# Kernel tuning notes

Hardware: AMD Instinct MI355X
Metric: run time of the kernel (lower is better)

## Reference

```python
import jax, jax.numpy as jnp
import numpy as np
from jax import lax

FX, FY = 518.857, 519.469   # NYU-v2 depth intrinsics (cx/cy unused by forward)
B, H, W = 8, 479, 639       # TRAIN_CROP_SIZE = [W, H]; H+1, W+1 divisible by 4
P = 8                       # even PATCH_SIZE -> box-filter output is [H+1, W+1]
EPS = 1e-6


def _coords():
    # u_u0 = x - W/2, v_v0 = y - H/2, broadcast over [B,1,H,W]
    u = jnp.arange(W, dtype=jnp.float32)[None, None, None, :] - W / 2.0
    v = jnp.arange(H, dtype=jnp.float32)[None, None, :, None] - H / 2.0
    return u, v


def _surface_normal(xyz):
    # xyz: [H, W, 3] -> normals [H, W, 3]
    x, y, z = xyz[..., 0], xyz[..., 1], xyz[..., 2]
    # 9 box-filtered moments in a single depthwise conv (the original does 9 conv2d calls)
    mom = jnp.stack([x * x, x * y, x * z, y * y, y * z, z * z, x, y, z], 0)[None]  # [1,9,H,W]
    kern = jnp.ones((9, 1, P, P), xyz.dtype)
    s = lax.conv_general_dilated(mom, kern, (1, 1), [(P // 2, P // 2)] * 2,
                                 feature_group_count=9)[0]  # [9, H+1, W+1]
    xx, xy, xz, yy, yz, zz, xs, ys, zs = s
    ATA = jnp.stack([xx, xy, xz, xy, yy, yz, xz, yz, zz], -1)  # [H+1, W+1, 9]
    Hp, Wp = ATA.shape[0], ATA.shape[1]
    ATA = ATA.reshape(Hp, Wp, 3, 3) + EPS * jnp.eye(3, dtype=xyz.dtype)
    AT1 = jnp.stack([xs, ys, zs], -1)[..., None]  # [H+1, W+1, 3, 1]
    # original loops over 4x4 sub-patches with overlap=0 -> equivalent full-grid solve
    n = jnp.linalg.solve(ATA, AT1)                # [H+1, W+1, 3, 1]
    n = n / jnp.sqrt(jnp.sum(n * n, axis=2, keepdims=True))
    n = n[:-1, :-1, :, 0]                         # [H, W, 3]
    # orient toward camera: flip where dot(n, xyz) > 0
    flip = jnp.sum(n * xyz, axis=2, keepdims=True) > 0
    return jnp.where(flip, -n, n)


def _fit_normals(depth):
    # depth: [B,1,H,W] -> surface normals [B,3,H,W], zeroed where depth <= 0
    u, v = _coords()
    x = u * depth / FX
    y = v * depth / FY
    xyz = jnp.concatenate([x, y, depth], 1).transpose(0, 2, 3, 1)  # [B,H,W,3]
    sn = jax.vmap(_surface_normal)(xyz).transpose(0, 3, 1, 2)      # [B,3,H,W]
    return jnp.where(depth > 0, sn, 0.0)


def setup_inputs() -> dict:
    key = jax.random.key(0)
    k1, k2 = jax.random.split(key)
    prediction = jax.random.uniform(k1, (B, 1, H, W), jnp.float32)
    gt = jax.random.uniform(k2, (B, 1, H, W), jnp.float32)
    return {"prediction": prediction, "gt": gt}


def reference(prediction, gt):
    return jnp.mean(jnp.abs(_fit_normals(prediction) - _fit_normals(gt)))
```

## Files before the change

kernel.cpp:

```cpp
#include <hip/hip_runtime.h>

#define HH 479
#define WW 639
#define BATCH 8
#define NACC 64


__device__ __forceinline__ void solve_normal(
    float xx, float xy, float xz, float yy, float yz, float zz,
    float xs, float ys, float zs,
    float a_c, float b_c, float d0,
    float* nx, float* ny, float* nz)
{
    const double EPSV = 1e-6;
    double p = (double)xx + EPSV, q = (double)xy, r = (double)xz;
    double s = (double)yy + EPSV, t = (double)yz, u = (double)zz + EPSV;
    double c00 = s * u - t * t;
    double c01 = r * t - q * u;
    double c02 = q * t - r * s;
    double c11 = p * u - r * r;
    double c12 = q * r - p * t;
    double c22 = p * s - q * q;
    double m0 = c00 * (double)xs + c01 * (double)ys + c02 * (double)zs;
    double m1 = c01 * (double)xs + c11 * (double)ys + c12 * (double)zs;
    double m2 = c02 * (double)xs + c12 * (double)ys + c22 * (double)zs;
    float f0 = (float)m0, f1 = (float)m1, f2 = (float)m2;
    float g = fmaf(f0, a_c, fmaf(f1, b_c, f2));
    float inv = rsqrtf(fmaf(f0, f0, fmaf(f1, f1, f2 * f2)));
    if (g > 0.0f) inv = -inv;
    if (!(d0 > 0.0f)) inv = 0.0f;
    *nx = f0 * inv; *ny = f1 * inv; *nz = f2 * inv;
}

__global__ __launch_bounds__(256, 4)
void ppal_main(const float* __restrict__ pred, const float* __restrict__ gt,
               double* __restrict__ acc)
{
    const int tx = threadIdx.x;
    const int ty = threadIdx.y;
    const int tid = ty * 16 + tx;
    const int j0 = blockIdx.x * 16;
    const int i0 = blockIdx.y * 16;
    const int b  = blockIdx.z;

    const float invFX = 1.0f / 518.857f;
    const float invFY = 1.0f / 519.469f;

    __shared__ float sd[2][23 * 24];
    __shared__ float cs[2][384][6];

    const float* src0 = pred + (size_t)b * (HH * WW);
    const float* src1 = gt   + (size_t)b * (HH * WW);
    for (int idx = tid; idx < 23 * 24; idx += 256) {
        int lr = idx / 24, lc = idx - lr * 24;
        int r = i0 - 4 + lr, c = j0 - 4 + lc;
        bool ok = (lc < 23) && (r >= 0) && (r < HH) && (c >= 0) && (c < WW);
        int off = r * WW + c;
        sd[0][idx] = ok ? src0[off] : 0.0f;
        sd[1][idx] = ok ? src1[off] : 0.0f;
    }
    __syncthreads();

    for (int t = tid; t < 384; t += 256) {
        int i = t / 24;
        int c = t - i * 24;
        float S1[2] = {0.f, 0.f}, Sb[2] = {0.f, 0.f}, Sbb[2] = {0.f, 0.f};
        float T1[2] = {0.f, 0.f}, Tb[2] = {0.f, 0.f};
#pragma unroll
        for (int dr = 0; dr < 8; ++dr) {
            float bv = ((float)(i0 + i - 4 + dr) - 239.5f) * invFY;
#pragma unroll
            for (int k = 0; k < 2; ++k) {
                float d  = sd[k][(i + dr) * 24 + c];
                float bd = bv * d;
                T1[k] += d;
                Tb[k] += bd;
                S1[k]  = fmaf(d,  d,  S1[k]);
                Sb[k]  = fmaf(bd, d,  Sb[k]);
                Sbb[k] = fmaf(bd, bd, Sbb[k]);
            }
        }
#pragma unroll
        for (int k = 0; k < 2; ++k) {
            float* e = cs[k][t];
            *(float2*)(e)     = make_float2(S1[k], Sb[k]);
            *(float2*)(e + 2) = make_float2(Sbb[k], T1[k]);
            e[4] = Tb[k];
        }
    }
    __syncthreads();

    const int i = i0 + ty, j = j0 + tx;
    const bool valid = (i < HH) && (j < WW);

    float contrib = 0.0f;
    if (valid) {
        float aa[8], a2[8];
#pragma unroll
        for (int dc = 0; dc < 8; ++dc) {
            float a = ((float)(j - 4 + dc) - 319.5f) * invFX;
            aa[dc] = a;
            a2[dc] = a * a;
        }
        float bc = ((float)i - 239.5f) * invFY;
        const int ebase = ty * 24 + tx;

        float n2[2][3];
#pragma unroll
        for (int k = 0; k < 2; ++k) {
            float xx = 0.f, xy = 0.f, xz = 0.f, yy = 0.f, yz = 0.f, zz = 0.f;
            float xs = 0.f, ys = 0.f, zs = 0.f;
#pragma unroll
            for (int dc = 0; dc < 8; ++dc) {
                const float* e = cs[k][ebase + dc];
                float2 p01 = *(const float2*)(e);
                float2 p23 = *(const float2*)(e + 2);
                float  tb  = e[4];
                zz += p01.x;  yz += p01.y;  yy += p23.x;
                zs += p23.y;  ys += tb;
                xz = fmaf(aa[dc], p01.x, xz);
                xy = fmaf(aa[dc], p01.y, xy);
                xs = fmaf(aa[dc], p23.y, xs);
                xx = fmaf(a2[dc], p01.x, xx);
            }
            float d0 = sd[k][(ty + 4) * 24 + (tx + 4)];
            solve_normal(xx, xy, xz, yy, yz, zz, xs, ys, zs,
                         aa[4], bc, d0, &n2[k][0], &n2[k][1], &n2[k][2]);
        }
        contrib = fabsf(n2[0][0] - n2[1][0])
                + fabsf(n2[0][1] - n2[1][1])
                + fabsf(n2[0][2] - n2[1][2]);
    }

    float v = contrib;
#pragma unroll
    for (int off = 32; off > 0; off >>= 1) v += __shfl_down(v, off, 64);
    __shared__ float wsum[4];
    int wid = tid >> 6, lane = tid & 63;
    if (lane == 0) wsum[wid] = v;
    __syncthreads();
    if (tid == 0) {
        double bs = (double)wsum[0] + (double)wsum[1] + (double)wsum[2] + (double)wsum[3];
        int slot = (blockIdx.x + 40 * blockIdx.y + 1200 * blockIdx.z) & (NACC - 1);
        atomicAdd(&acc[slot], bs);
    }
}

__global__ void ppal_finalize(const double* __restrict__ acc, float* __restrict__ out)
{
    int lane = threadIdx.x;
    double v = acc[lane];
#pragma unroll
    for (int off = 32; off > 0; off >>= 1) v += __shfl_down(v, off, 64);
    if (lane == 0)
        out[0] = (float)(v * (1.0 / 7345944.0));
}

extern "C" void kernel_launch(void* const* d_in, const int* in_sizes, int n_in,
                              void* d_out, int out_size, void* d_ws, size_t ws_size,
                              hipStream_t stream)
{
    const float* pred = (const float*)d_in[0];
    const float* gt   = (const float*)d_in[1];
    float* out  = (float*)d_out;
    double* acc = (double*)d_ws;

    hipMemsetAsync(acc, 0, NACC * sizeof(double), stream);

    dim3 grid((WW + 15) / 16, (HH + 15) / 16, BATCH);
    dim3 block(16, 16);
    ppal_main<<<grid, block, 0, stream>>>(pred, gt, acc);
    ppal_finalize<<<1, 64, 0, stream>>>(acc, out);
}
```

Before: 104.8 us.

## Solve normals in centered fp32 instead of fp64 and pad shared records

Replaces the double-precision cofactor solve with a single-precision one that first centers the moment matrix (subtracting the outer product of the means over 64 samples), which keeps the cofactors well conditioned in fp32. This avoids slow fp64 arithmetic on the per-pixel critical path. It also pads the shared-memory column-sum records with two extra floats every 16 entries, to reduce LDS bank conflicts on the strided float2 reads. The centering changes the solved vector, relying on normalization and sign flipping to give the same normal direction, and the EPS regularization now applies to the centered matrix, so small numerical differences from the reference are possible.

```diff
diff --git a/kernel.cpp b/kernel.cpp
--- a/kernel.cpp
+++ b/kernel.cpp
@@ -12,25 +12,32 @@
     float a_c, float b_c, float d0,
     float* nx, float* ny, float* nz)
 {
-    const double EPSV = 1e-6;
-    double p = (double)xx + EPSV, q = (double)xy, r = (double)xz;
-    double s = (double)yy + EPSV, t = (double)yz, u = (double)zz + EPSV;
-    double c00 = s * u - t * t;
-    double c01 = r * t - q * u;
-    double c02 = q * t - r * s;
-    double c11 = p * u - r * r;
-    double c12 = q * r - p * t;
-    double c22 = p * s - q * q;
-    double m0 = c00 * (double)xs + c01 * (double)ys + c02 * (double)zs;
-    double m1 = c01 * (double)xs + c11 * (double)ys + c12 * (double)zs;
-    double m2 = c02 * (double)xs + c12 * (double)ys + c22 * (double)zs;
-    float f0 = (float)m0, f1 = (float)m1, f2 = (float)m2;
-    float g = fmaf(f0, a_c, fmaf(f1, b_c, f2));
-    float inv = rsqrtf(fmaf(f0, f0, fmaf(f1, f1, f2 * f2)));
+    const float EPSV = 1e-6f;
+    const float inv64 = 1.0f / 64.0f;
+    float hx = xs * inv64, hy = ys * inv64, hz = zs * inv64;
+    float cxx = fmaf(-hx, xs, xx) + EPSV;
+    float cxy = fmaf(-hx, ys, xy);
+    float cxz = fmaf(-hx, zs, xz);
+    float cyy = fmaf(-hy, ys, yy) + EPSV;
+    float cyz = fmaf(-hy, zs, yz);
+    float czz = fmaf(-hz, zs, zz) + EPSV;
+    float c00 = fmaf(cyy, czz, -cyz * cyz);
+    float c01 = fmaf(cxz, cyz, -cxy * czz);
+    float c02 = fmaf(cxy, cyz, -cxz * cyy);
+    float c11 = fmaf(cxx, czz, -cxz * cxz);
+    float c12 = fmaf(cxy, cxz, -cxx * cyz);
+    float c22 = fmaf(cxx, cyy, -cxy * cxy);
+    float m0 = fmaf(c00, xs, fmaf(c01, ys, c02 * zs));
+    float m1 = fmaf(c01, xs, fmaf(c11, ys, c12 * zs));
+    float m2 = fmaf(c02, xs, fmaf(c12, ys, c22 * zs));
+    float g  = fmaf(m0, a_c, fmaf(m1, b_c, m2));
+    float inv = rsqrtf(fmaf(m0, m0, fmaf(m1, m1, m2 * m2)));
     if (g > 0.0f) inv = -inv;
     if (!(d0 > 0.0f)) inv = 0.0f;
-    *nx = f0 * inv; *ny = f1 * inv; *nz = f2 * inv;
+    *nx = m0 * inv; *ny = m1 * inv; *nz = m2 * inv;
 }
+
+__device__ __forceinline__ int rec_addr(int t) { return 6 * t + 2 * (t >> 4); }
 
 __global__ __launch_bounds__(256, 4)
 void ppal_main(const float* __restrict__ pred, const float* __restrict__ gt,
@@ -47,7 +54,7 @@
     const float invFY = 1.0f / 519.469f;
 
     __shared__ float sd[2][23 * 24];
-    __shared__ float cs[2][384][6];
+    __shared__ float cs[2][6 * 384 + 2 * 24];
 
     const float* src0 = pred + (size_t)b * (HH * WW);
     const float* src1 = gt   + (size_t)b * (HH * WW);
@@ -80,9 +87,10 @@
                 Sbb[k] = fmaf(bd, bd, Sbb[k]);
             }
         }
+        int ra = rec_addr(t);
 #pragma unroll
         for (int k = 0; k < 2; ++k) {
-            float* e = cs[k][t];
+            float* e = &cs[k][ra];
             *(float2*)(e)     = make_float2(S1[k], Sb[k]);
             *(float2*)(e + 2) = make_float2(Sbb[k], T1[k]);
             e[4] = Tb[k];
@@ -112,7 +120,7 @@
             float xs = 0.f, ys = 0.f, zs = 0.f;
 #pragma unroll
             for (int dc = 0; dc < 8; ++dc) {
-                const float* e = cs[k][ebase + dc];
+                const float* e = &cs[k][rec_addr(ebase + dc)];
                 float2 p01 = *(const float2*)(e);
                 float2 p23 = *(const float2*)(e + 2);
                 float  tb  = e[4];
```

Result: slower. 115.8 us (+10.6%).
